# Kernel optimization log

Measured on AMD Instinct MI355X. Metric: run time of the kernel, lower is better.

## Reference

```python
import jax, jax.numpy as jnp
import numpy as np

B, D3, DQ, H, UNITS, SK = 32, 1024, 1024, 1024, 1024, 1024


def setup_inputs() -> dict:
    key = jax.random.key(0)
    ks = jax.random.split(key, 11)
    return {
        "K": jax.random.normal(ks[0], (B, SK, UNITS), jnp.float32),
        "Q": jax.random.normal(ks[1], (B, DQ, D3), jnp.float32),
        "M": jax.random.normal(ks[2], (B, D3, D3), jnp.float32),
        "ht": jax.random.normal(ks[3], (B, D3, H), jnp.float32),
        "Wp": jax.random.normal(ks[4], (D3, DQ), jnp.float32) * 0.02,
        "bp": jax.random.normal(ks[5], (D3,), jnp.float32) * 0.02,
        "W3": jax.random.normal(ks[6], (D3, D3), jnp.float32) * 0.02,
        "W4": jax.random.normal(ks[7], (D3, D3), jnp.float32) * 0.02,
        "b3": jax.random.normal(ks[8], (D3,), jnp.float32) * 0.02,
        "Wd": jax.random.normal(ks[9], (H + D3, UNITS), jnp.float32) * 0.02,
        "bd": jax.random.normal(ks[10], (UNITS,), jnp.float32) * 0.02,
    }


def reference(K, Q, M, ht, Wp, bp, W3, W4, b3, Wd, bd):
    # q = Wp @ Q + bp  -> (B, d3, d3); bp broadcasts over the last axis
    q = jnp.einsum('ij,bjk->bik', Wp, Q) + bp
    # concat([ht, q], axis=-1) -> (B, d3, h + d3), then fresh Dense(units)
    concat = jnp.concatenate([ht, q], axis=-1)
    mlp = jnp.einsum('bdc,cu->bdu', concat, Wd) + bd  # (B, d3, units)
    # scores = K @ mlp^T, softmax over last axis (computed but unused in the
    # original layer's output -- kept for faithfulness; DCE'd under jit)
    scores = jnp.einsum('bsu,bdu->bsd', K, mlp)       # (B, sK, d3)
    distribution = jax.nn.softmax(scores, axis=-1)
    del distribution
    # Belta = relu(W3 @ M + W4 @ q + b3), gated multiply with q
    Belta = jax.nn.relu(
        jnp.einsum('ij,bjk->bik', W3, M)
        + jnp.einsum('ij,bjk->bik', W4, q)
        + b3
    )
    q_new = Belta * q  # (B, d3, d3)
    return q_new
```

## Files before the change

### kernel.cpp

```cpp
#include <hip/hip_runtime.h>
#include <stdint.h>


#define D_ 1024

typedef __attribute__((ext_vector_type(8))) short short8;
typedef __attribute__((ext_vector_type(4))) float floatx4;
typedef __attribute__((ext_vector_type(4))) unsigned short us4;

#define VMCNT0() asm volatile("s_waitcnt vmcnt(0)" ::: "memory")
#define LGKM0()  asm volatile("s_waitcnt lgkmcnt(0)" ::: "memory")

__device__ __forceinline__ unsigned short f2bf(float f) {
  union { float f; unsigned int u; } v; v.f = f;
  unsigned int u = v.u;
  unsigned int r = (u + 0x7FFFu + ((u >> 16) & 1u)) >> 16;
  return (unsigned short)r;
}

__device__ __forceinline__ float bf2f(unsigned short h) {
  union { unsigned int u; float f; } v; v.u = ((unsigned int)h) << 16;
  return v.f;
}

__device__ __forceinline__ void async_load16(const void* g, void* l) {
  __builtin_amdgcn_global_load_lds(
      (const __attribute__((address_space(1))) unsigned int*)g,
      (__attribute__((address_space(3))) unsigned int*)l, 16, 0, 0);
}

__global__ __launch_bounds__(256) void transpose_cvt(
    const float* __restrict__ in, unsigned short* __restrict__ out) {
  __shared__ float tile[64][65];
  const int b = blockIdx.z;
  const long base = ((long)b) << 20;
  const int r0 = blockIdx.y * 64, c0 = blockIdx.x * 64;
  const int t = threadIdx.x;
  const int tr = t >> 4, tc4 = (t & 15) * 4;
#pragma unroll
  for (int p = 0; p < 4; ++p) {
    const int row = p * 16 + tr;
    const float4 v = *(const float4*)&in[base + (long)(r0 + row) * D_ + c0 + tc4];
    tile[row][tc4 + 0] = v.x; tile[row][tc4 + 1] = v.y;
    tile[row][tc4 + 2] = v.z; tile[row][tc4 + 3] = v.w;
  }
  __syncthreads();
#pragma unroll
  for (int p = 0; p < 4; ++p) {
    const int c = p * 16 + tr;
    us4 pk;
    pk.x = f2bf(tile[tc4 + 0][c]);
    pk.y = f2bf(tile[tc4 + 1][c]);
    pk.z = f2bf(tile[tc4 + 2][c]);
    pk.w = f2bf(tile[tc4 + 3][c]);
    *(us4*)&out[base + (long)(c0 + c) * D_ + r0 + tc4] = pk;
  }
}

__global__ __launch_bounds__(256) void convert_weights(
    const float* __restrict__ Wp, const float* __restrict__ W3,
    const float* __restrict__ W4, unsigned short* __restrict__ Wpb,
    unsigned short* __restrict__ A2) {
  const int i = blockIdx.x * 256 + threadIdx.x;
  const long e = (long)i * 4;
  const int row = (int)(e >> 10);
  const int col = (int)(e & 1023);
  const float4 a = ((const float4*)Wp)[i];
  us4 pa; pa.x = f2bf(a.x); pa.y = f2bf(a.y); pa.z = f2bf(a.z); pa.w = f2bf(a.w);
  ((us4*)Wpb)[i] = pa;
  const float4 w3 = ((const float4*)W3)[i];
  us4 p3; p3.x = f2bf(w3.x); p3.y = f2bf(w3.y); p3.z = f2bf(w3.z); p3.w = f2bf(w3.w);
  *(us4*)&A2[(long)row * 2048 + col] = p3;
  const float4 w4 = ((const float4*)W4)[i];
  us4 p4; p4.x = f2bf(w4.x); p4.y = f2bf(w4.y); p4.z = f2bf(w4.z); p4.w = f2bf(w4.w);
  *(us4*)&A2[(long)row * 2048 + 1024 + col] = p4;
}

template <int NT, int LDA, bool IS_G2>
__global__ __launch_bounds__(512, 2) void gemm8p(
    const unsigned short* __restrict__ A,
    const unsigned short* __restrict__ B1,
    const unsigned short* __restrict__ B2,
    const float* __restrict__ bias,
    void* __restrict__ outp) {
  __shared__ __align__(16) unsigned short As[2][256 * 64];
  __shared__ __align__(16) unsigned short Bs[2][256 * 64];

  const int lane = threadIdx.x & 63;
  const int w = threadIdx.x >> 6;
  const int wm = (w >> 2) * 128;
  const int wn = (w & 3) * 64;
  const int l15 = lane & 15;
  const int quad = lane >> 4;

  const int bid = blockIdx.x;
  const int swz = (bid & 7) * 64 + (bid >> 3);
  const int b = swz >> 4;
  const int m0 = ((swz >> 2) & 3) * 256;
  const int n0 = (swz & 3) * 256;
  const long bb = ((long)b) << 20;

  const int sr = lane >> 3;
  const int sc = ((lane & 7) ^ sr) * 8;

  const unsigned short* Ag = A + (long)(m0 + w * 16 + sr) * LDA + sc;
  const unsigned short* Bg1 = B1 + bb + (long)(n0 + w * 16 + sr) * D_ + sc;
  const unsigned short* Bg2 =
      B2 ? (B2 + bb + (long)(n0 + w * 16 + sr) * D_ + sc) : (const unsigned short*)0;

  const int kx0 = (quad * 16) ^ ((lane & 7) << 4);
  const int kx1 = (64 + quad * 16) ^ ((lane & 7) << 4);

  floatx4 acc[8][4] = {};

  auto stageA = [&](int buf, int kt) {
#pragma unroll
    for (int h = 0; h < 2; ++h)
#pragma unroll
      for (int j = 0; j < 2; ++j)
        async_load16(Ag + (long)(h * 128 + j * 8) * LDA + (long)kt * 64,
                     &As[buf][(h * 128 + w * 16 + j * 8) * 64]);
  };
  auto stageB = [&](int buf, int kt) {
    const unsigned short* bs;
    if constexpr (IS_G2) {
      bs = (kt < 16) ? (Bg1 + (long)kt * 64) : (Bg2 + (long)(kt - 16) * 64);
    } else {
      bs = Bg1 + (long)kt * 64;
    }
#pragma unroll
    for (int h = 0; h < 2; ++h)
#pragma unroll
      for (int j = 0; j < 2; ++j)
        async_load16(bs + (long)(h * 128 + j * 8) * D_,
                     &Bs[buf][(h * 128 + w * 16 + j * 8) * 64]);
  };

  auto ldA = [&](int buf, int fi, int kx) -> short8 {
    return *(const short8*)((const char*)&As[buf][0] +
                            (long)((wm + fi * 16 + l15) * 128 + kx));
  };
  auto ldB = [&](int buf, int fi, int kx) -> short8 {
    return *(const short8*)((const char*)&Bs[buf][0] +
                            (long)((wn + fi * 16 + l15) * 128 + kx));
  };

  stageA(0, 0);
  stageB(0, 0);
  VMCNT0();
  __builtin_amdgcn_s_barrier();

  short8 a[4][2], bq[2][2];

  auto tile = [&](int t, int buf, bool st) {
#pragma unroll
    for (int r = 0; r < 4; ++r) { a[r][0] = ldA(buf, r, kx0); a[r][1] = ldA(buf, r, kx1); }
#pragma unroll
    for (int c = 0; c < 2; ++c) { bq[c][0] = ldB(buf, c, kx0); bq[c][1] = ldB(buf, c, kx1); }
    if (st) stageA(buf ^ 1, t + 1);
    __builtin_amdgcn_s_barrier();
    LGKM0();
    __builtin_amdgcn_sched_barrier(0);
    __builtin_amdgcn_s_setprio(1);
#pragma unroll
    for (int r = 0; r < 4; ++r)
#pragma unroll
      for (int c = 0; c < 2; ++c)
#pragma unroll
        for (int ks = 0; ks < 2; ++ks)
          acc[r][c] = __builtin_amdgcn_mfma_f32_16x16x32_bf16(
              a[r][ks], bq[c][ks], acc[r][c], 0, 0, 0);
    __builtin_amdgcn_s_setprio(0);
    __builtin_amdgcn_s_barrier();

#pragma unroll
    for (int c = 0; c < 2; ++c) { bq[c][0] = ldB(buf, 2 + c, kx0); bq[c][1] = ldB(buf, 2 + c, kx1); }
    if (st) stageB(buf ^ 1, t + 1);
    __builtin_amdgcn_s_barrier();
    LGKM0();
    __builtin_amdgcn_sched_barrier(0);
    __builtin_amdgcn_s_setprio(1);
#pragma unroll
    for (int r = 0; r < 4; ++r)
#pragma unroll
      for (int c = 0; c < 2; ++c)
#pragma unroll
        for (int ks = 0; ks < 2; ++ks)
          acc[r][2 + c] = __builtin_amdgcn_mfma_f32_16x16x32_bf16(
              a[r][ks], bq[c][ks], acc[r][2 + c], 0, 0, 0);
    __builtin_amdgcn_s_setprio(0);
    __builtin_amdgcn_s_barrier();

#pragma unroll
    for (int r = 0; r < 4; ++r) { a[r][0] = ldA(buf, 4 + r, kx0); a[r][1] = ldA(buf, 4 + r, kx1); }
    __builtin_amdgcn_s_barrier();
    LGKM0();
    __builtin_amdgcn_sched_barrier(0);
    __builtin_amdgcn_s_setprio(1);
#pragma unroll
    for (int r = 0; r < 4; ++r)
#pragma unroll
      for (int c = 0; c < 2; ++c)
#pragma unroll
        for (int ks = 0; ks < 2; ++ks)
          acc[4 + r][2 + c] = __builtin_amdgcn_mfma_f32_16x16x32_bf16(
              a[r][ks], bq[c][ks], acc[4 + r][2 + c], 0, 0, 0);
    __builtin_amdgcn_s_setprio(0);
    __builtin_amdgcn_s_barrier();

#pragma unroll
    for (int c = 0; c < 2; ++c) { bq[c][0] = ldB(buf, c, kx0); bq[c][1] = ldB(buf, c, kx1); }
    __builtin_amdgcn_s_barrier();
    LGKM0();
    __builtin_amdgcn_sched_barrier(0);
    __builtin_amdgcn_s_setprio(1);
#pragma unroll
    for (int r = 0; r < 4; ++r)
#pragma unroll
      for (int c = 0; c < 2; ++c)
#pragma unroll
        for (int ks = 0; ks < 2; ++ks)
          acc[4 + r][c] = __builtin_amdgcn_mfma_f32_16x16x32_bf16(
              a[r][ks], bq[c][ks], acc[4 + r][c], 0, 0, 0);
    __builtin_amdgcn_s_setprio(0);
    VMCNT0();
    __builtin_amdgcn_s_barrier();
  };

#pragma unroll 1
  for (int tt = 0; tt < NT; tt += 2) {
    tile(tt, 0, true);
    tile(tt + 1, 1, tt + 2 < NT);
  }

  if constexpr (!IS_G2) {
    unsigned short* qt = (unsigned short*)outp;
#pragma unroll
    for (int c = 0; c < 4; ++c) {
      const int col = n0 + wn + c * 16 + l15;
      const float bv = bias[col];
#pragma unroll
      for (int r = 0; r < 8; ++r) {
        const int row = m0 + wm + r * 16 + quad * 4;
        const floatx4 v = acc[r][c];
        us4 pk;
        pk.x = f2bf(v.x + bv); pk.y = f2bf(v.y + bv);
        pk.z = f2bf(v.z + bv); pk.w = f2bf(v.w + bv);
        *(us4*)&qt[bb + (long)col * D_ + row] = pk;
      }
    }
  } else {
    float* outv = (float*)outp;
#pragma unroll
    for (int c = 0; c < 4; ++c) {
      const int col = n0 + wn + c * 16 + l15;
      const float bv = bias[col];
#pragma unroll
      for (int r = 0; r < 8; ++r) {
        const int row = m0 + wm + r * 16 + quad * 4;
        const floatx4 v = acc[r][c];
        const us4 qv = *(const us4*)&B2[bb + (long)col * D_ + row];
        outv[bb + (long)(row + 0) * D_ + col] = fmaxf(v.x + bv, 0.0f) * bf2f(qv.x);
        outv[bb + (long)(row + 1) * D_ + col] = fmaxf(v.y + bv, 0.0f) * bf2f(qv.y);
        outv[bb + (long)(row + 2) * D_ + col] = fmaxf(v.z + bv, 0.0f) * bf2f(qv.z);
        outv[bb + (long)(row + 3) * D_ + col] = fmaxf(v.w + bv, 0.0f) * bf2f(qv.w);
      }
    }
  }
}

extern "C" void kernel_launch(void* const* d_in, const int* in_sizes, int n_in,
                              void* d_out, int out_size, void* d_ws, size_t ws_size,
                              hipStream_t stream) {
  const float* Q  = (const float*)d_in[1];
  const float* M  = (const float*)d_in[2];
  const float* Wp = (const float*)d_in[4];
  const float* bp = (const float*)d_in[5];
  const float* W3 = (const float*)d_in[6];
  const float* W4 = (const float*)d_in[7];
  const float* b3 = (const float*)d_in[8];
  float* out = (float*)d_out;

  char* ws = (char*)d_ws;
  unsigned short* qt  = (unsigned short*)(ws);
  unsigned short* Qt  = (unsigned short*)(ws + (64l  << 20));
  unsigned short* Mt  = (unsigned short*)(ws + (128l << 20));
  unsigned short* Wpb = (unsigned short*)(ws + (192l << 20));
  unsigned short* A2  = (unsigned short*)(ws + (194l << 20));

  dim3 tgrid(16, 16, 32);
  transpose_cvt<<<tgrid, 256, 0, stream>>>(Q, Qt);
  transpose_cvt<<<tgrid, 256, 0, stream>>>(M, Mt);
  convert_weights<<<1024, 256, 0, stream>>>(Wp, W3, W4, Wpb, A2);

  gemm8p<16, 1024, false><<<dim3(512), dim3(512), 0, stream>>>(
      Wpb, Qt, (const unsigned short*)nullptr, bp, qt);
  gemm8p<32, 2048, true><<<dim3(512), dim3(512), 0, stream>>>(
      A2, Mt, qt, b3, out);
}
```

Measured before the change: 680.5 us.

## Prefetch B two tiles ahead, split staging, and merge transpose launches

Restructures the GEMM main loop so B tiles are staged two k-steps ahead while A is staged one ahead. Staging is split into half-tile chunks spread across the MFMA phases, and the end-of-tile wait becomes a partial vmcnt(4) instead of a full drain. It also keeps all four B fragments in registers, which removes one LDS reload and barrier phase per tile. The two transpose-convert launches are merged into a single launch with a doubled grid. The risks are more register pressure and subtle LDS buffer hazards from writing B into the current buffer while it may still be read.

```diff
diff --git a/kernel.cpp b/kernel.cpp
--- a/kernel.cpp
+++ b/kernel.cpp
@@ -9,6 +9,7 @@
 typedef __attribute__((ext_vector_type(4))) unsigned short us4;
 
 #define VMCNT0() asm volatile("s_waitcnt vmcnt(0)" ::: "memory")
+#define VMCNT4() asm volatile("s_waitcnt vmcnt(4)" ::: "memory")
 #define LGKM0()  asm volatile("s_waitcnt lgkmcnt(0)" ::: "memory")
 
 __device__ __forceinline__ unsigned short f2bf(float f) {
@@ -29,10 +30,14 @@
       (__attribute__((address_space(3))) unsigned int*)l, 16, 0, 0);
 }
 
-__global__ __launch_bounds__(256) void transpose_cvt(
-    const float* __restrict__ in, unsigned short* __restrict__ out) {
+__global__ __launch_bounds__(256) void transpose_cvt2(
+    const float* __restrict__ in0, unsigned short* __restrict__ out0,
+    const float* __restrict__ in1, unsigned short* __restrict__ out1) {
   __shared__ float tile[64][65];
-  const int b = blockIdx.z;
+  const int zz = blockIdx.z;
+  const float* in = (zz < 32) ? in0 : in1;
+  unsigned short* out = (zz < 32) ? out0 : out1;
+  const int b = zz & 31;
   const long base = ((long)b) << 20;
   const int r0 = blockIdx.y * 64, c0 = blockIdx.x * 64;
   const int t = threadIdx.x;
@@ -113,15 +118,13 @@
 
   floatx4 acc[8][4] = {};
 
-  auto stageA = [&](int buf, int kt) {
-#pragma unroll
-    for (int h = 0; h < 2; ++h)
-#pragma unroll
-      for (int j = 0; j < 2; ++j)
-        async_load16(Ag + (long)(h * 128 + j * 8) * LDA + (long)kt * 64,
-                     &As[buf][(h * 128 + w * 16 + j * 8) * 64]);
-  };
-  auto stageB = [&](int buf, int kt) {
+  auto stageAh = [&](int buf, int kt, int h) {
+#pragma unroll
+    for (int j = 0; j < 2; ++j)
+      async_load16(Ag + (long)(h * 128 + j * 8) * LDA + (long)kt * 64,
+                   &As[buf][(h * 128 + w * 16 + j * 8) * 64]);
+  };
+  auto stageBh = [&](int buf, int kt, int h) {
     const unsigned short* bs;
     if constexpr (IS_G2) {
       bs = (kt < 16) ? (Bg1 + (long)kt * 64) : (Bg2 + (long)(kt - 16) * 64);
@@ -129,11 +132,9 @@
       bs = Bg1 + (long)kt * 64;
     }
 #pragma unroll
-    for (int h = 0; h < 2; ++h)
-#pragma unroll
-      for (int j = 0; j < 2; ++j)
-        async_load16(bs + (long)(h * 128 + j * 8) * D_,
-                     &Bs[buf][(h * 128 + w * 16 + j * 8) * 64]);
+    for (int j = 0; j < 2; ++j)
+      async_load16(bs + (long)(h * 128 + j * 8) * D_,
+                   &Bs[buf][(h * 128 + w * 16 + j * 8) * 64]);
   };
 
   auto ldA = [&](int buf, int fi, int kx) -> short8 {
@@ -145,19 +146,20 @@
                             (long)((wn + fi * 16 + l15) * 128 + kx));
   };
 
-  stageA(0, 0);
-  stageB(0, 0);
-  VMCNT0();
+  stageAh(0, 0, 0); stageAh(0, 0, 1);
+  stageBh(0, 0, 0); stageBh(0, 0, 1);
+  stageBh(1, 1, 0); stageBh(1, 1, 1);
+  VMCNT4();
   __builtin_amdgcn_s_barrier();
 
-  short8 a[4][2], bq[2][2];
-
-  auto tile = [&](int t, int buf, bool st) {
+  short8 a[4][2], bq[4][2];
+
+  auto tile = [&](int t, int buf) {
 #pragma unroll
     for (int r = 0; r < 4; ++r) { a[r][0] = ldA(buf, r, kx0); a[r][1] = ldA(buf, r, kx1); }
 #pragma unroll
     for (int c = 0; c < 2; ++c) { bq[c][0] = ldB(buf, c, kx0); bq[c][1] = ldB(buf, c, kx1); }
-    if (st) stageA(buf ^ 1, t + 1);
+    if (t + 1 < NT) stageAh(buf ^ 1, t + 1, 0);
     __builtin_amdgcn_s_barrier();
     LGKM0();
     __builtin_amdgcn_sched_barrier(0);
@@ -174,8 +176,8 @@
     __builtin_amdgcn_s_barrier();
 
 #pragma unroll
-    for (int c = 0; c < 2; ++c) { bq[c][0] = ldB(buf, 2 + c, kx0); bq[c][1] = ldB(buf, 2 + c, kx1); }
-    if (st) stageB(buf ^ 1, t + 1);
+    for (int c = 0; c < 2; ++c) { bq[2 + c][0] = ldB(buf, 2 + c, kx0); bq[2 + c][1] = ldB(buf, 2 + c, kx1); }
+    if (t + 1 < NT) stageAh(buf ^ 1, t + 1, 1);
     __builtin_amdgcn_s_barrier();
     LGKM0();
     __builtin_amdgcn_sched_barrier(0);
@@ -187,12 +189,13 @@
 #pragma unroll
         for (int ks = 0; ks < 2; ++ks)
           acc[r][2 + c] = __builtin_amdgcn_mfma_f32_16x16x32_bf16(
-              a[r][ks], bq[c][ks], acc[r][2 + c], 0, 0, 0);
+              a[r][ks], bq[2 + c][ks], acc[r][2 + c], 0, 0, 0);
     __builtin_amdgcn_s_setprio(0);
     __builtin_amdgcn_s_barrier();
 
 #pragma unroll
     for (int r = 0; r < 4; ++r) { a[r][0] = ldA(buf, 4 + r, kx0); a[r][1] = ldA(buf, 4 + r, kx1); }
+    if (t + 2 < NT) stageBh(buf, t + 2, 0);
     __builtin_amdgcn_s_barrier();
     LGKM0();
     __builtin_amdgcn_sched_barrier(0);
@@ -204,15 +207,12 @@
 #pragma unroll
         for (int ks = 0; ks < 2; ++ks)
           acc[4 + r][2 + c] = __builtin_amdgcn_mfma_f32_16x16x32_bf16(
-              a[r][ks], bq[c][ks], acc[4 + r][2 + c], 0, 0, 0);
-    __builtin_amdgcn_s_setprio(0);
-    __builtin_amdgcn_s_barrier();
-
-#pragma unroll
-    for (int c = 0; c < 2; ++c) { bq[c][0] = ldB(buf, c, kx0); bq[c][1] = ldB(buf, c, kx1); }
-    __builtin_amdgcn_s_barrier();
-    LGKM0();
-    __builtin_amdgcn_sched_barrier(0);
+              a[r][ks], bq[2 + c][ks], acc[4 + r][2 + c], 0, 0, 0);
+    __builtin_amdgcn_s_setprio(0);
+    __builtin_amdgcn_s_barrier();
+
+    if (t + 2 < NT) stageBh(buf, t + 2, 1);
+    __builtin_amdgcn_s_barrier();
     __builtin_amdgcn_s_setprio(1);
 #pragma unroll
     for (int r = 0; r < 4; ++r)
@@ -223,14 +223,14 @@
           acc[4 + r][c] = __builtin_amdgcn_mfma_f32_16x16x32_bf16(
               a[r][ks], bq[c][ks], acc[4 + r][c], 0, 0, 0);
     __builtin_amdgcn_s_setprio(0);
-    VMCNT0();
+    if (t < NT - 2) { VMCNT4(); } else { VMCNT0(); }
     __builtin_amdgcn_s_barrier();
   };
 
 #pragma unroll 1
   for (int tt = 0; tt < NT; tt += 2) {
-    tile(tt, 0, true);
-    tile(tt + 1, 1, tt + 2 < NT);
+    tile(tt, 0);
+    tile(tt + 1, 1);
   }
 
   if constexpr (!IS_G2) {
@@ -288,9 +288,8 @@
   unsigned short* Wpb = (unsigned short*)(ws + (192l << 20));
   unsigned short* A2  = (unsigned short*)(ws + (194l << 20));
 
-  dim3 tgrid(16, 16, 32);
-  transpose_cvt<<<tgrid, 256, 0, stream>>>(Q, Qt);
-  transpose_cvt<<<tgrid, 256, 0, stream>>>(M, Mt);
+  dim3 tgrid(16, 16, 64);
+  transpose_cvt2<<<tgrid, 256, 0, stream>>>(Q, Qt, M, Mt);
   convert_weights<<<1024, 256, 0, stream>>>(Wp, W3, W4, Wpb, A2);
 
   gemm8p<16, 1024, false><<<dim3(512), dim3(512), 0, stream>>>(
```

Result: no change. 689.1 us (+1.3%).
